# Kernel optimization log

Hardware: AMD Instinct MI355X
Metric: run time of the kernel (lower is better)

## Reference

```python
import jax, jax.numpy as jnp
import numpy as np

B = 32768
IN = 2
H = 512
OUT = 1
OM = 128   # output_module_size
HG = 128   # halt_gate_size
MAX_ITER = 32
EPS = 1e-3


def _w(k, shape, fan_in):
    bound = 1.0 / np.sqrt(fan_in)
    return jax.random.uniform(k, shape, jnp.float32, -bound, bound)


def setup_inputs() -> dict:
    key = jax.random.key(0)
    ks = jax.random.split(key, 32)
    d = {"x": jax.random.normal(ks[0], (B, IN), jnp.float32)}
    # four LSTM gates: input Linear(IN,H) and hidden Linear(H,H), each with bias
    names = ["i", "f", "c", "o"]
    for j, g in enumerate(names):
        d[f"W{g}_x"] = _w(ks[1 + 4 * j], (IN, H), IN)
        d[f"b{g}_x"] = _w(ks[2 + 4 * j], (H,), IN)
        d[f"W{g}_h"] = _w(ks[3 + 4 * j], (H, H), H)
        d[f"b{g}_h"] = _w(ks[4 + 4 * j], (H,), H)
    # halt gate: Linear(H,HG) -> ReLU -> Linear(HG,1) -> Sigmoid
    d["halt_W1"] = _w(ks[17], (H, HG), H)
    d["halt_b1"] = _w(ks[18], (HG,), H)
    d["halt_W2"] = _w(ks[19], (HG, 1), HG)
    d["halt_b2"] = _w(ks[20], (1,), HG)
    # output module: Linear(H,OM) -> ReLU -> Linear(OM,OM) -> Linear(OM,OUT) -> Sigmoid
    d["out_W1"] = _w(ks[21], (H, OM), H)
    d["out_b1"] = _w(ks[22], (OM,), H)
    d["out_W2"] = _w(ks[23], (OM, OM), OM)
    d["out_b2"] = _w(ks[24], (OM,), OM)
    d["out_W3"] = _w(ks[25], (OM, OUT), OM)
    d["out_b3"] = _w(ks[26], (OUT,), OM)
    return d


def _act_forward(x, Wi_x, bi_x, Wi_h, bi_h, Wf_x, bf_x, Wf_h, bf_h,
                 Wc_x, bc_x, Wc_h, bc_h, Wo_x, bo_x, Wo_h, bo_h,
                 halt_W1, halt_b1, halt_W2, halt_b2,
                 out_W1, out_b1, out_W2, out_b2, out_W3, out_b3):
    b = x.shape[0]
    # input projections are iteration-invariant: precompute once
    xi = x @ Wi_x + bi_x
    xf = x @ Wf_x + bf_x
    xc = x @ Wc_x + bc_x
    xo = x @ Wo_x + bo_x

    def step(carry, t):
        state, cell, p_sum, active, acc = carry
        i_g = jax.nn.sigmoid(xi + state @ Wi_h + bi_h)
        f_g = jax.nn.sigmoid(xf + state @ Wf_h + bf_h)
        c_g = jnp.tanh(xc + state @ Wc_h + bc_h)
        o_g = jax.nn.sigmoid(xo + state @ Wo_h + bo_h)
        am = active[:, None]
        new_cell = jnp.where(am, f_g * cell + i_g * c_g, cell)
        new_state = jnp.where(am, o_g * jnp.tanh(new_cell), state)
        # output head (inactive rows contribute zero weight below)
        h1 = jax.nn.relu(new_state @ out_W1 + out_b1)
        out = jax.nn.sigmoid((h1 @ out_W2 + out_b2) @ out_W3 + out_b3)  # [B,OUT]
        # halt probability
        hh = jax.nn.relu(new_state @ halt_W1 + halt_b1)
        halt = jax.nn.sigmoid(hh @ halt_W2 + halt_b2)[:, 0]  # [B]
        halt = jnp.where(active, halt, 0.0)
        p_new = p_sum + halt
        is_last = t == (MAX_ITER - 1)
        finished = (p_new >= 1.0 - EPS) | is_last
        adj = active & finished
        halt_adj = jnp.where(adj, halt + (1.0 - p_new), halt)
        p_new = jnp.where(adj, 1.0, p_new)
        acc = acc + out * halt_adj[:, None]
        active_new = active & jnp.logical_not(finished)
        return (new_state, new_cell, p_new, active_new, acc), None

    init = (
        jnp.zeros((b, H), jnp.float32),   # state
        jnp.zeros((b, H), jnp.float32),   # cell
        jnp.zeros((b,), jnp.float32),     # p_sum
        jnp.ones((b,), bool),             # active
        jnp.zeros((b, OUT), jnp.float32), # weighted-output accumulator
    )
    (state, cell, p_sum, active, acc), _ = jax.lax.scan(step, init, jnp.arange(MAX_ITER))
    return acc


def reference(x, Wi_x, bi_x, Wi_h, bi_h, Wf_x, bf_x, Wf_h, bf_h,
              Wc_x, bc_x, Wc_h, bc_h, Wo_x, bo_x, Wo_h, bo_h,
              halt_W1, halt_b1, halt_W2, halt_b2,
              out_W1, out_b1, out_W2, out_b2, out_W3, out_b3):
    return _act_forward(x, Wi_x, bi_x, Wi_h, bi_h, Wf_x, bf_x, Wf_h, bf_h,
                        Wc_x, bc_x, Wc_h, bc_h, Wo_x, bo_x, Wo_h, bo_h,
                        halt_W1, halt_b1, halt_W2, halt_b2,
                        out_W1, out_b1, out_W2, out_b2, out_W3, out_b3)
```

## Files before the change

### kernel.cpp

```cpp
#include <hip/hip_runtime.h>
#include <hip/hip_bf16.h>

#define KD   544
#define ASTR 552
#define RPB  64
#define THR  512
#define T1   3
#define NROW 32768

typedef __bf16 bf8 __attribute__((ext_vector_type(8)));
typedef float f32x4 __attribute__((ext_vector_type(4)));

__device__ __forceinline__ float sigm(float x)  { return 1.0f / (1.0f + __expf(-x)); }
__device__ __forceinline__ float tanh_(float x) { return 2.0f / (1.0f + __expf(-2.0f * x)) - 1.0f; }

__global__ void pack_all(const float* __restrict__ Wi_h, const float* __restrict__ Wf_h,
                         const float* __restrict__ Wc_h, const float* __restrict__ Wo_h,
                         const float* __restrict__ Wi_x, const float* __restrict__ Wf_x,
                         const float* __restrict__ Wc_x, const float* __restrict__ Wo_x,
                         const float* __restrict__ bi_x, const float* __restrict__ bf_x,
                         const float* __restrict__ bc_x, const float* __restrict__ bo_x,
                         const float* __restrict__ bi_h, const float* __restrict__ bf_h,
                         const float* __restrict__ bc_h, const float* __restrict__ bo_h,
                         const float* __restrict__ outW1, const float* __restrict__ outb1,
                         const float* __restrict__ haltW1, const float* __restrict__ haltb1,
                         const float* __restrict__ outW2, const float* __restrict__ outb2,
                         const float* __restrict__ outW3, const float* __restrict__ outb3,
                         __bf16* __restrict__ whT, __bf16* __restrict__ w1cat,
                         float* __restrict__ w23, float* __restrict__ b23,
                         int* __restrict__ cntp)
{
  int b = blockIdx.x;
  if (b < 4352) {
    int idx = b * 256 + threadIdx.x;
    int j = idx / KD, k = idx % KD;
    int g = j >> 9, c = j & 511;
    const float* Wh = (g == 0) ? Wi_h : (g == 1) ? Wf_h : (g == 2) ? Wc_h : Wo_h;
    const float* Wx = (g == 0) ? Wi_x : (g == 1) ? Wf_x : (g == 2) ? Wc_x : Wo_x;
    const float* bx = (g == 0) ? bi_x : (g == 1) ? bf_x : (g == 2) ? bc_x : bo_x;
    const float* bh = (g == 0) ? bi_h : (g == 1) ? bf_h : (g == 2) ? bc_h : bo_h;
    float v = 0.0f;
    if (k < 512)       v = Wh[k * 512 + c];
    else if (k == 512) v = Wx[c];
    else if (k == 513) v = Wx[512 + c];
    else if (k == 514) v = bx[c] + bh[c];
    whT[idx] = (__bf16)v;
  } else if (b < 4896) {
    int idx = (b - 4352) * 256 + threadIdx.x;
    int j = idx / KD, k = idx % KD;
    float v = 0.0f;
    if (j < 128) {
      if (k < 512)       v = outW1[k * 128 + j];
      else if (k == 514) v = outb1[j];
    } else {
      int jj = j - 128;
      if (k < 512)       v = haltW1[k * 128 + jj];
      else if (k == 514) v = haltb1[jj];
    }
    w1cat[idx] = (__bf16)v;
  } else {
    int c1 = threadIdx.x;
    if (c1 < 128) {
      float s = 0.0f;
      for (int c2 = 0; c2 < 128; ++c2) s += outW2[c1 * 128 + c2] * outW3[c2];
      w23[c1] = s;
    }
    if (c1 == 0) {
      float bb = 0.0f;
      for (int c2 = 0; c2 < 128; ++c2) bb += outb2[c2] * outW3[c2];
      b23[0] = bb + outb3[0];
      cntp[0] = 0;
    }
  }
}

template<bool P1>
__global__ __launch_bounds__(THR, 2) void act_pass(
    const float* __restrict__ x,
    const __bf16* __restrict__ whT,
    const __bf16* __restrict__ w1cat,
    const float* __restrict__ w23,
    const float* __restrict__ b23p,
    const float* __restrict__ haltW2,
    const float* __restrict__ haltb2,
    __bf16* __restrict__ sstate,
    __bf16* __restrict__ scell,
    float* __restrict__ spsum,
    float* __restrict__ saccum,
    int* __restrict__ sidx,
    int* __restrict__ cntp,
    float* __restrict__ out)
{
  int cnt_v = 0, sbase = 0;
  if constexpr (!P1) {
    cnt_v = cntp[0];
    sbase = blockIdx.x * RPB;
    if (sbase >= cnt_v) return;
  }

  __shared__ __align__(16) __bf16 Abuf[2][RPB][ASTR];
  __shared__ float wv[256];
  __shared__ float partials[8][RPB];
  __shared__ int anyact_s;
  __shared__ int rowslot[RPB];

  const int tid  = threadIdx.x;
  const int wave = tid >> 6;
  const int lane = tid & 63;
  const int lg   = lane >> 4;
  const int lc   = lane & 15;
  const int row0 = blockIdx.x * RPB;

  if (tid < 256) wv[tid] = (tid < 128) ? w23[tid] : haltW2[tid - 128];

  if constexpr (P1) {
    for (int w = tid; w < 2 * RPB * 69; w += THR) {
      int bb  = w / (RPB * 69);
      int rem = w - bb * (RPB * 69);
      int r   = rem / 69;
      int j   = rem - r * 69;
      bf8 v;
#pragma unroll
      for (int e = 0; e < 8; ++e) v[e] = (__bf16)0.0f;
      if (j == 64) {
        v[0] = (__bf16)x[(row0 + r) * 2 + 0];
        v[1] = (__bf16)x[(row0 + r) * 2 + 1];
        v[2] = (__bf16)1.0f;
      }
      *(bf8*)&Abuf[bb][r][j * 8] = v;
    }
  } else {
    for (int w = tid; w < RPB * 68; w += THR) {
      int r = w / 68, j = w - r * 68;
      int slot = sbase + r;
      bf8 v;
#pragma unroll
      for (int e = 0; e < 8; ++e) v[e] = (__bf16)0.0f;
      if (slot < cnt_v) v = *(const bf8*)(sstate + (size_t)slot * KD + j * 8);
      *(bf8*)&Abuf[0][r][j * 8] = v;
      if (j >= 64) *(bf8*)&Abuf[1][r][j * 8] = v;
    }
    for (int w = tid; w < RPB * 64; w += THR) {
      int r = w / 64, j = w - r * 64;
      int slot = sbase + r;
      bf8 v;
#pragma unroll
      for (int e = 0; e < 8; ++e) v[e] = (__bf16)0.0f;
      if (slot < cnt_v) v = *(const bf8*)(scell + (size_t)slot * 512 + j * 8);
      *(bf8*)&Abuf[1][r][j * 8] = v;
    }
  }
  if (tid == 0) anyact_s = 1;
  __syncthreads();

  float cell[4][4][4];
  if constexpr (P1) {
#pragma unroll
    for (int n = 0; n < 4; ++n)
#pragma unroll
      for (int m = 0; m < 4; ++m)
#pragma unroll
        for (int q = 0; q < 4; ++q) cell[n][m][q] = 0.0f;
  } else {
#pragma unroll
    for (int n = 0; n < 4; ++n)
#pragma unroll
      for (int m = 0; m < 4; ++m)
#pragma unroll
        for (int q = 0; q < 4; ++q)
          cell[n][m][q] = (float)Abuf[1][m * 16 + lg * 4 + q][wave * 64 + n * 16 + lc];
  }

  bool  valid, active;
  float p_sum, accum;
  int   oidx;
  if constexpr (P1) {
    valid = (tid < 64); active = valid;
    p_sum = 0.0f; accum = 0.0f; oidx = row0 + tid;
  } else {
    int slot = sbase + tid;
    valid = (tid < 64) && (slot < cnt_v);
    active = valid;
    p_sum = valid ? spsum[slot]  : 1.0f;
    accum = valid ? saccum[slot] : 0.0f;
    oidx  = valid ? sidx[slot]   : 0;
    __syncthreads();
  }

  const float b23 = b23p[0];
  const float bh2 = haltb2[0];
  const f32x4 zero4 = {0.0f, 0.0f, 0.0f, 0.0f};

  int cur = 0;
  const int T0 = P1 ? 0 : T1;
  const int TE = P1 ? T1 : 32;
  for (int t = T0; t < TE; ++t) {
    const int kstart = (P1 && t == 0) ? 16 : 0;
#pragma unroll
    for (int n = 0; n < 4; ++n) {
      const int colb = wave * 64 + n * 16 + lc;
      const __bf16* bp0 = whT + (size_t)(colb)        * KD + lg * 8;
      const __bf16* bp1 = whT + (size_t)(512  + colb) * KD + lg * 8;
      const __bf16* bp2 = whT + (size_t)(1024 + colb) * KD + lg * 8;
      const __bf16* bp3 = whT + (size_t)(1536 + colb) * KD + lg * 8;
      f32x4 acc[4][4];
#pragma unroll
      for (int g = 0; g < 4; ++g)
#pragma unroll
        for (int m = 0; m < 4; ++m) acc[g][m] = zero4;

      bf8 b0 = *(const bf8*)(bp0 + kstart * 32);
      bf8 b1 = *(const bf8*)(bp1 + kstart * 32);
      bf8 b2 = *(const bf8*)(bp2 + kstart * 32);
      bf8 b3 = *(const bf8*)(bp3 + kstart * 32);
#pragma unroll 1
      for (int kk = kstart; kk < 16; ++kk) {
        bf8 av[4];
#pragma unroll
        for (int m = 0; m < 4; ++m)
          av[m] = *(const bf8*)&Abuf[cur][m * 16 + lc][kk * 32 + lg * 8];
        bf8 nb0 = *(const bf8*)(bp0 + (kk + 1) * 32);
        bf8 nb1 = *(const bf8*)(bp1 + (kk + 1) * 32);
        bf8 nb2 = *(const bf8*)(bp2 + (kk + 1) * 32);
        bf8 nb3 = *(const bf8*)(bp3 + (kk + 1) * 32);
#pragma unroll
        for (int m = 0; m < 4; ++m) {
          acc[0][m] = __builtin_amdgcn_mfma_f32_16x16x32_bf16(av[m], b0, acc[0][m], 0, 0, 0);
          acc[1][m] = __builtin_amdgcn_mfma_f32_16x16x32_bf16(av[m], b1, acc[1][m], 0, 0, 0);
          acc[2][m] = __builtin_amdgcn_mfma_f32_16x16x32_bf16(av[m], b2, acc[2][m], 0, 0, 0);
          acc[3][m] = __builtin_amdgcn_mfma_f32_16x16x32_bf16(av[m], b3, acc[3][m], 0, 0, 0);
        }
        b0 = nb0; b1 = nb1; b2 = nb2; b3 = nb3;
      }
      {
        bf8 av[4];
#pragma unroll
        for (int m = 0; m < 4; ++m)
          av[m] = *(const bf8*)&Abuf[cur][m * 16 + lc][16 * 32 + lg * 8];
#pragma unroll
        for (int m = 0; m < 4; ++m) {
          acc[0][m] = __builtin_amdgcn_mfma_f32_16x16x32_bf16(av[m], b0, acc[0][m], 0, 0, 0);
          acc[1][m] = __builtin_amdgcn_mfma_f32_16x16x32_bf16(av[m], b1, acc[1][m], 0, 0, 0);
          acc[2][m] = __builtin_amdgcn_mfma_f32_16x16x32_bf16(av[m], b2, acc[2][m], 0, 0, 0);
          acc[3][m] = __builtin_amdgcn_mfma_f32_16x16x32_bf16(av[m], b3, acc[3][m], 0, 0, 0);
        }
      }
#pragma unroll
      for (int m = 0; m < 4; ++m) {
#pragma unroll
        for (int q = 0; q < 4; ++q) {
          float iv = sigm(acc[0][m][q]);
          float fv = sigm(acc[1][m][q]);
          float cv = tanh_(acc[2][m][q]);
          float ov = sigm(acc[3][m][q]);
          float cn = fv * cell[n][m][q] + iv * cv;
          cell[n][m][q] = cn;
          float h = ov * tanh_(cn);
          Abuf[cur ^ 1][m * 16 + lg * 4 + q][colb] = (__bf16)h;
        }
      }
    }
    __syncthreads();
    {
      const int jb0 = wave * 32 + lc;
      const __bf16* hp0 = w1cat + (size_t)jb0        * KD + lg * 8;
      const __bf16* hp1 = w1cat + (size_t)(jb0 + 16) * KD + lg * 8;
      f32x4 hacc[2][4];
#pragma unroll
      for (int n2 = 0; n2 < 2; ++n2)
#pragma unroll
        for (int m = 0; m < 4; ++m) hacc[n2][m] = zero4;
      bf8 hb0 = *(const bf8*)(hp0);
      bf8 hb1 = *(const bf8*)(hp1);
#pragma unroll 1
      for (int kk = 0; kk < 16; ++kk) {
        bf8 av[4];
#pragma unroll
        for (int m = 0; m < 4; ++m)
          av[m] = *(const bf8*)&Abuf[cur ^ 1][m * 16 + lc][kk * 32 + lg * 8];
        bf8 nb0 = *(const bf8*)(hp0 + (kk + 1) * 32);
        bf8 nb1 = *(const bf8*)(hp1 + (kk + 1) * 32);
#pragma unroll
        for (int m = 0; m < 4; ++m) {
          hacc[0][m] = __builtin_amdgcn_mfma_f32_16x16x32_bf16(av[m], hb0, hacc[0][m], 0, 0, 0);
          hacc[1][m] = __builtin_amdgcn_mfma_f32_16x16x32_bf16(av[m], hb1, hacc[1][m], 0, 0, 0);
        }
        hb0 = nb0; hb1 = nb1;
      }
      {
        bf8 av[4];
#pragma unroll
        for (int m = 0; m < 4; ++m)
          av[m] = *(const bf8*)&Abuf[cur ^ 1][m * 16 + lc][16 * 32 + lg * 8];
#pragma unroll
        for (int m = 0; m < 4; ++m) {
          hacc[0][m] = __builtin_amdgcn_mfma_f32_16x16x32_bf16(av[m], hb0, hacc[0][m], 0, 0, 0);
          hacc[1][m] = __builtin_amdgcn_mfma_f32_16x16x32_bf16(av[m], hb1, hacc[1][m], 0, 0, 0);
        }
      }
      const float wv0 = wv[wave * 32 + lc];
      const float wv1 = wv[wave * 32 + 16 + lc];
#pragma unroll
      for (int m = 0; m < 4; ++m) {
#pragma unroll
        for (int q = 0; q < 4; ++q) {
          float s = fmaxf(hacc[0][m][q], 0.0f) * wv0 + fmaxf(hacc[1][m][q], 0.0f) * wv1;
          s += __shfl_xor(s, 1, 64);
          s += __shfl_xor(s, 2, 64);
          s += __shfl_xor(s, 4, 64);
          s += __shfl_xor(s, 8, 64);
          if (lc == 0) partials[wave][m * 16 + lg * 4 + q] = s;
        }
      }
    }
    __syncthreads();
    if (tid < 64) {
      float od = partials[0][tid] + partials[1][tid] + partials[2][tid] + partials[3][tid] + b23;
      float hd = partials[4][tid] + partials[5][tid] + partials[6][tid] + partials[7][tid] + bh2;
      float outv  = sigm(od);
      float haltv = sigm(hd);
      if (active) {
        float pn  = p_sum + haltv;
        bool  fin = (pn >= 0.999f) || (t == 31);
        accum += outv * (fin ? (haltv + (1.0f - pn)) : haltv);
        p_sum  = fin ? 1.0f : pn;
        active = !fin;
      }
      unsigned long long mk = __ballot(active);
      if (tid == 0) anyact_s = (mk != 0ull) ? 1 : 0;
    }
    __syncthreads();
    if (!anyact_s) break;
    cur ^= 1;
  }

  if constexpr (P1) {
    if (tid < 64) {
      unsigned long long mk = __ballot(active);
      int base = 0;
      if (lane == 0 && mk) base = atomicAdd(cntp, __popcll(mk));
      base = __shfl(base, 0, 64);
      int rank = __popcll(mk & ((1ull << lane) - 1ull));
      int slot = active ? (base + rank) : -1;
      rowslot[tid] = slot;
      if (active) {
        spsum[slot]  = p_sum;
        saccum[slot] = accum;
        sidx[slot]   = oidx;
      } else {
        out[oidx] = accum;
      }
      if (tid == 0) anyact_s = (mk != 0ull) ? 1 : 0;
    }
    __syncthreads();
    if (anyact_s) {
#pragma unroll
      for (int n = 0; n < 4; ++n)
#pragma unroll
        for (int m = 0; m < 4; ++m)
#pragma unroll
          for (int q = 0; q < 4; ++q)
            Abuf[cur ^ 1][m * 16 + lg * 4 + q][wave * 64 + n * 16 + lc] = (__bf16)cell[n][m][q];
      __syncthreads();
      for (int w = tid; w < RPB * 132; w += THR) {
        int r = w / 132, j = w - r * 132;
        int slot = rowslot[r];
        if (slot < 0) continue;
        if (j < 68)
          *(bf8*)(sstate + (size_t)slot * KD + j * 8) = *(const bf8*)&Abuf[cur][r][j * 8];
        else {
          int jj = j - 68;
          *(bf8*)(scell + (size_t)slot * 512 + jj * 8) = *(const bf8*)&Abuf[cur ^ 1][r][jj * 8];
        }
      }
    }
  } else {
    if (valid) out[oidx] = accum;
  }
}

extern "C" void kernel_launch(void* const* d_in, const int* in_sizes, int n_in,
                              void* d_out, int out_size, void* d_ws, size_t ws_size,
                              hipStream_t stream) {
  const float* x     = (const float*)d_in[0];
  const float* Wi_x  = (const float*)d_in[1];
  const float* bi_x  = (const float*)d_in[2];
  const float* Wi_h  = (const float*)d_in[3];
  const float* bi_h  = (const float*)d_in[4];
  const float* Wf_x  = (const float*)d_in[5];
  const float* bf_x  = (const float*)d_in[6];
  const float* Wf_h  = (const float*)d_in[7];
  const float* bf_h  = (const float*)d_in[8];
  const float* Wc_x  = (const float*)d_in[9];
  const float* bc_x  = (const float*)d_in[10];
  const float* Wc_h  = (const float*)d_in[11];
  const float* bc_h  = (const float*)d_in[12];
  const float* Wo_x  = (const float*)d_in[13];
  const float* bo_x  = (const float*)d_in[14];
  const float* Wo_h  = (const float*)d_in[15];
  const float* bo_h  = (const float*)d_in[16];
  const float* hW1   = (const float*)d_in[17];
  const float* hb1   = (const float*)d_in[18];
  const float* hW2   = (const float*)d_in[19];
  const float* hb2   = (const float*)d_in[20];
  const float* oW1   = (const float*)d_in[21];
  const float* ob1   = (const float*)d_in[22];
  const float* oW2   = (const float*)d_in[23];
  const float* ob2   = (const float*)d_in[24];
  const float* oW3   = (const float*)d_in[25];
  const float* ob3   = (const float*)d_in[26];

  char* p = (char*)d_ws;
  __bf16* whT   = (__bf16*)p;                       p += (size_t)2048 * KD * 2;
  __bf16* w1cat = (__bf16*)p;                       p += (size_t)256 * KD * 2;
  float*  w23   = (float*)p;                        p += 512;
  float*  b23   = (float*)p;                        p += 16;
  int*    cnt   = (int*)p;                          p += 240;
  __bf16* sstate= (__bf16*)p;                       p += (size_t)NROW * KD * 2;
  __bf16* scell = (__bf16*)p;                       p += (size_t)NROW * 512 * 2;
  float*  spsum = (float*)p;                        p += (size_t)NROW * 4;
  float*  saccum= (float*)p;                        p += (size_t)NROW * 4;
  int*    sidx  = (int*)p;                          p += (size_t)NROW * 4;

  pack_all<<<dim3(4897), dim3(256), 0, stream>>>(
      Wi_h, Wf_h, Wc_h, Wo_h, Wi_x, Wf_x, Wc_x, Wo_x,
      bi_x, bf_x, bc_x, bo_x, bi_h, bf_h, bc_h, bo_h,
      oW1, ob1, hW1, hb1, oW2, ob2, oW3, ob3,
      whT, w1cat, w23, b23, cnt);
  act_pass<true><<<dim3(NROW / RPB), dim3(THR), 0, stream>>>(
      x, whT, w1cat, w23, b23, hW2, hb2,
      sstate, scell, spsum, saccum, sidx, cnt, (float*)d_out);
  act_pass<false><<<dim3(NROW / RPB), dim3(THR), 0, stream>>>(
      x, whT, w1cat, w23, b23, hW2, hb2,
      sstate, scell, spsum, saccum, sidx, cnt, (float*)d_out);
}
```

Before: 407.3 us.

## Tile-transpose weight packing via LDS and deepen MFMA operand prefetch to two stages

The weight-packing kernel now transposes 64x64 tiles through shared memory, giving coalesced reads and vectorized bf16 writes, and launches far fewer blocks. The gate and head GEMM loops now prefetch B operands two K-steps ahead and A operands one step ahead, with the tail step folded into the main loop. This is meant to cut the strided-read cost of packing and to hide global and LDS load latency behind the MFMAs. The cost is more live registers, which could hurt occupancy at two blocks per CU, plus redundant clamped loads at the tail.

```diff
diff --git a/kernel.cpp b/kernel.cpp
--- a/kernel.cpp
+++ b/kernel.cpp
@@ -30,36 +30,84 @@
                          float* __restrict__ w23, float* __restrict__ b23,
                          int* __restrict__ cntp)
 {
-  int b = blockIdx.x;
-  if (b < 4352) {
-    int idx = b * 256 + threadIdx.x;
-    int j = idx / KD, k = idx % KD;
-    int g = j >> 9, c = j & 511;
+  __shared__ float tile[64][65];
+  const int b = blockIdx.x;
+  const int tid = threadIdx.x;
+
+  if (b < 256) {
+    const int g = b >> 6, ct = (b >> 3) & 7, kt = b & 7;
+    const int c0 = ct * 64, k0 = kt * 64;
     const float* Wh = (g == 0) ? Wi_h : (g == 1) ? Wf_h : (g == 2) ? Wc_h : Wo_h;
+    const int ty = tid >> 6, tx = tid & 63;
+#pragma unroll
+    for (int r = 0; r < 16; ++r) {
+      int kl = r * 4 + ty;
+      tile[kl][tx] = Wh[(size_t)(k0 + kl) * 512 + c0 + tx];
+    }
+    __syncthreads();
+    const int jj = tid >> 2, kq = tid & 3;
+    bf8 lo, hi;
+#pragma unroll
+    for (int i = 0; i < 8; ++i) lo[i] = (__bf16)tile[kq * 16 + i][jj];
+#pragma unroll
+    for (int i = 0; i < 8; ++i) hi[i] = (__bf16)tile[kq * 16 + 8 + i][jj];
+    __bf16* dst = whT + (size_t)(g * 512 + c0 + jj) * KD + k0 + kq * 16;
+    *(bf8*)dst = lo;
+    *(bf8*)(dst + 8) = hi;
+  } else if (b < 288) {
+    const int b2 = b - 256;
+    const int g = b2 >> 3, ct = b2 & 7;
     const float* Wx = (g == 0) ? Wi_x : (g == 1) ? Wf_x : (g == 2) ? Wc_x : Wo_x;
     const float* bx = (g == 0) ? bi_x : (g == 1) ? bf_x : (g == 2) ? bc_x : bo_x;
     const float* bh = (g == 0) ? bi_h : (g == 1) ? bf_h : (g == 2) ? bc_h : bo_h;
-    float v = 0.0f;
-    if (k < 512)       v = Wh[k * 512 + c];
-    else if (k == 512) v = Wx[c];
-    else if (k == 513) v = Wx[512 + c];
-    else if (k == 514) v = bx[c] + bh[c];
-    whT[idx] = (__bf16)v;
-  } else if (b < 4896) {
-    int idx = (b - 4352) * 256 + threadIdx.x;
-    int j = idx / KD, k = idx % KD;
-    float v = 0.0f;
-    if (j < 128) {
-      if (k < 512)       v = outW1[k * 128 + j];
-      else if (k == 514) v = outb1[j];
-    } else {
-      int jj = j - 128;
-      if (k < 512)       v = haltW1[k * 128 + jj];
-      else if (k == 514) v = haltb1[jj];
-    }
-    w1cat[idx] = (__bf16)v;
+    const int jj = tid >> 2, kq = tid & 3;
+    const int c = ct * 64 + jj;
+    bf8 v;
+#pragma unroll
+    for (int i = 0; i < 8; ++i) {
+      int k = 512 + kq * 8 + i;
+      float f = 0.0f;
+      if (k == 512)      f = Wx[c];
+      else if (k == 513) f = Wx[512 + c];
+      else if (k == 514) f = bx[c] + bh[c];
+      v[i] = (__bf16)f;
+    }
+    *(bf8*)(whT + (size_t)(g * 512 + c) * KD + 512 + kq * 8) = v;
+  } else if (b < 320) {
+    const int b2 = b - 288;
+    const int src = b2 >> 4, jt = (b2 >> 3) & 1, kt = b2 & 7;
+    const float* W = src ? haltW1 : outW1;
+    const int c0 = jt * 64, k0 = kt * 64;
+    const int ty = tid >> 6, tx = tid & 63;
+#pragma unroll
+    for (int r = 0; r < 16; ++r) {
+      int kl = r * 4 + ty;
+      tile[kl][tx] = W[(size_t)(k0 + kl) * 128 + c0 + tx];
+    }
+    __syncthreads();
+    const int jj = tid >> 2, kq = tid & 3;
+    bf8 lo, hi;
+#pragma unroll
+    for (int i = 0; i < 8; ++i) lo[i] = (__bf16)tile[kq * 16 + i][jj];
+#pragma unroll
+    for (int i = 0; i < 8; ++i) hi[i] = (__bf16)tile[kq * 16 + 8 + i][jj];
+    __bf16* dst = w1cat + (size_t)(src * 128 + c0 + jj) * KD + k0 + kq * 16;
+    *(bf8*)dst = lo;
+    *(bf8*)(dst + 8) = hi;
+  } else if (b < 324) {
+    const int b2 = b - 320;
+    const int jj = tid >> 2, kq = tid & 3;
+    const int j = b2 * 64 + jj;
+    const float bias = (j < 128) ? outb1[j] : haltb1[j - 128];
+    bf8 v;
+#pragma unroll
+    for (int i = 0; i < 8; ++i) {
+      int k = 512 + kq * 8 + i;
+      v[i] = (__bf16)((k == 514) ? bias : 0.0f);
+    }
+    *(bf8*)(w1cat + (size_t)j * KD + 512 + kq * 8) = v;
   } else {
-    int c1 = threadIdx.x;
+    const int c1 = tid;
     if (c1 < 128) {
       float s = 0.0f;
       for (int c2 = 0; c2 < 128; ++c2) s += outW2[c1 * 128 + c2] * outW3[c2];
@@ -199,51 +247,49 @@
 #pragma unroll
     for (int n = 0; n < 4; ++n) {
       const int colb = wave * 64 + n * 16 + lc;
-      const __bf16* bp0 = whT + (size_t)(colb)        * KD + lg * 8;
-      const __bf16* bp1 = whT + (size_t)(512  + colb) * KD + lg * 8;
-      const __bf16* bp2 = whT + (size_t)(1024 + colb) * KD + lg * 8;
-      const __bf16* bp3 = whT + (size_t)(1536 + colb) * KD + lg * 8;
+      const __bf16* bp[4];
+      bp[0] = whT + (size_t)colb * KD + lg * 8;
+      bp[1] = bp[0] + (size_t)512  * KD;
+      bp[2] = bp[0] + (size_t)1024 * KD;
+      bp[3] = bp[0] + (size_t)1536 * KD;
       f32x4 acc[4][4];
 #pragma unroll
       for (int g = 0; g < 4; ++g)
 #pragma unroll
         for (int m = 0; m < 4; ++m) acc[g][m] = zero4;
 
-      bf8 b0 = *(const bf8*)(bp0 + kstart * 32);
-      bf8 b1 = *(const bf8*)(bp1 + kstart * 32);
-      bf8 b2 = *(const bf8*)(bp2 + kstart * 32);
-      bf8 b3 = *(const bf8*)(bp3 + kstart * 32);
+      bf8 bA[4], bB[4], avA[4];
+      const int k1 = (kstart < 16) ? kstart + 1 : 16;
+#pragma unroll
+      for (int g = 0; g < 4; ++g) {
+        bA[g] = *(const bf8*)(bp[g] + kstart * 32);
+        bB[g] = *(const bf8*)(bp[g] + k1 * 32);
+      }
+#pragma unroll
+      for (int m = 0; m < 4; ++m)
+        avA[m] = *(const bf8*)&Abuf[cur][m * 16 + lc][kstart * 32 + lg * 8];
+
 #pragma unroll 1
-      for (int kk = kstart; kk < 16; ++kk) {
-        bf8 av[4];
+      for (int kk = kstart; kk <= 16; ++kk) {
+        const int kp2 = (kk + 2 <= 16) ? kk + 2 : 16;
+        const int kp1 = (kk + 1 <= 16) ? kk + 1 : 16;
+        bf8 bC[4], avB[4];
+#pragma unroll
+        for (int g = 0; g < 4; ++g) bC[g] = *(const bf8*)(bp[g] + kp2 * 32);
 #pragma unroll
         for (int m = 0; m < 4; ++m)
-          av[m] = *(const bf8*)&Abuf[cur][m * 16 + lc][kk * 32 + lg * 8];
-        bf8 nb0 = *(const bf8*)(bp0 + (kk + 1) * 32);
-        bf8 nb1 = *(const bf8*)(bp1 + (kk + 1) * 32);
-        bf8 nb2 = *(const bf8*)(bp2 + (kk + 1) * 32);
-        bf8 nb3 = *(const bf8*)(bp3 + (kk + 1) * 32);
+          avB[m] = *(const bf8*)&Abuf[cur][m * 16 + lc][kp1 * 32 + lg * 8];
 #pragma unroll
         for (int m = 0; m < 4; ++m) {
-          acc[0][m] = __builtin_amdgcn_mfma_f32_16x16x32_bf16(av[m], b0, acc[0][m], 0, 0, 0);
-          acc[1][m] = __builtin_amdgcn_mfma_f32_16x16x32_bf16(av[m], b1, acc[1][m], 0, 0, 0);
-          acc[2][m] = __builtin_amdgcn_mfma_f32_16x16x32_bf16(av[m], b2, acc[2][m], 0, 0, 0);
-          acc[3][m] = __builtin_amdgcn_mfma_f32_16x16x32_bf16(av[m], b3, acc[3][m], 0, 0, 0);
+          acc[0][m] = __builtin_amdgcn_mfma_f32_16x16x32_bf16(avA[m], bA[0], acc[0][m], 0, 0, 0);
+          acc[1][m] = __builtin_amdgcn_mfma_f32_16x16x32_bf16(avA[m], bA[1], acc[1][m], 0, 0, 0);
+          acc[2][m] = __builtin_amdgcn_mfma_f32_16x16x32_bf16(avA[m], bA[2], acc[2][m], 0, 0, 0);
+          acc[3][m] = __builtin_amdgcn_mfma_f32_16x16x32_bf16(avA[m], bA[3], acc[3][m], 0, 0, 0);
         }
-        b0 = nb0; b1 = nb1; b2 = nb2; b3 = nb3;
-      }
-      {
-        bf8 av[4];
-#pragma unroll
-        for (int m = 0; m < 4; ++m)
-          av[m] = *(const bf8*)&Abuf[cur][m * 16 + lc][16 * 32 + lg * 8];
-#pragma unroll
-        for (int m = 0; m < 4; ++m) {
-          acc[0][m] = __builtin_amdgcn_mfma_f32_16x16x32_bf16(av[m], b0, acc[0][m], 0, 0, 0);
-          acc[1][m] = __builtin_amdgcn_mfma_f32_16x16x32_bf16(av[m], b1, acc[1][m], 0, 0, 0);
-          acc[2][m] = __builtin_amdgcn_mfma_f32_16x16x32_bf16(av[m], b2, acc[2][m], 0, 0, 0);
-          acc[3][m] = __builtin_amdgcn_mfma_f32_16x16x32_bf16(av[m], b3, acc[3][m], 0, 0, 0);
-        }
+#pragma unroll
+        for (int g = 0; g < 4; ++g) { bA[g] = bB[g]; bB[g] = bC[g]; }
+#pragma unroll
+        for (int m = 0; m < 4; ++m) avA[m] = avB[m];
       }
 #pragma unroll
       for (int m = 0; m < 4; ++m) {
@@ -263,40 +309,44 @@
     __syncthreads();
     {
       const int jb0 = wave * 32 + lc;
-      const __bf16* hp0 = w1cat + (size_t)jb0        * KD + lg * 8;
-      const __bf16* hp1 = w1cat + (size_t)(jb0 + 16) * KD + lg * 8;
+      const __bf16* hp[2];
+      hp[0] = w1cat + (size_t)jb0 * KD + lg * 8;
+      hp[1] = hp[0] + (size_t)16 * KD;
       f32x4 hacc[2][4];
 #pragma unroll
       for (int n2 = 0; n2 < 2; ++n2)
 #pragma unroll
         for (int m = 0; m < 4; ++m) hacc[n2][m] = zero4;
-      bf8 hb0 = *(const bf8*)(hp0);
-      bf8 hb1 = *(const bf8*)(hp1);
+
+      bf8 hA[2], hB[2], avA[4];
+#pragma unroll
+      for (int g = 0; g < 2; ++g) {
+        hA[g] = *(const bf8*)(hp[g]);
+        hB[g] = *(const bf8*)(hp[g] + 32);
+      }
+#pragma unroll
+      for (int m = 0; m < 4; ++m)
+        avA[m] = *(const bf8*)&Abuf[cur ^ 1][m * 16 + lc][lg * 8];
+
 #pragma unroll 1
-      for (int kk = 0; kk < 16; ++kk) {
-        bf8 av[4];
+      for (int kk = 0; kk <= 16; ++kk) {
+        const int kp2 = (kk + 2 <= 16) ? kk + 2 : 16;
+        const int kp1 = (kk + 1 <= 16) ? kk + 1 : 16;
+        bf8 hC[2], avB[4];
+#pragma unroll
+        for (int g = 0; g < 2; ++g) hC[g] = *(const bf8*)(hp[g] + kp2 * 32);
 #pragma unroll
         for (int m = 0; m < 4; ++m)
-          av[m] = *(const bf8*)&Abuf[cur ^ 1][m * 16 + lc][kk * 32 + lg * 8];
-        bf8 nb0 = *(const bf8*)(hp0 + (kk + 1) * 32);
-        bf8 nb1 = *(const bf8*)(hp1 + (kk + 1) * 32);
+          avB[m] = *(const bf8*)&Abuf[cur ^ 1][m * 16 + lc][kp1 * 32 + lg * 8];
 #pragma unroll
         for (int m = 0; m < 4; ++m) {
-          hacc[0][m] = __builtin_amdgcn_mfma_f32_16x16x32_bf16(av[m], hb0, hacc[0][m], 0, 0, 0);
-          hacc[1][m] = __builtin_amdgcn_mfma_f32_16x16x32_bf16(av[m], hb1, hacc[1][m], 0, 0, 0);
+          hacc[0][m] = __builtin_amdgcn_mfma_f32_16x16x32_bf16(avA[m], hA[0], hacc[0][m], 0, 0, 0);
+          hacc[1][m] = __builtin_amdgcn_mfma_f32_16x16x32_bf16(avA[m], hA[1], hacc[1][m], 0, 0, 0);
         }
-        hb0 = nb0; hb1 = nb1;
-      }
-      {
-        bf8 av[4];
-#pragma unroll
-        for (int m = 0; m < 4; ++m)
-          av[m] = *(const bf8*)&Abuf[cur ^ 1][m * 16 + lc][16 * 32 + lg * 8];
-#pragma unroll
-        for (int m = 0; m < 4; ++m) {
-          hacc[0][m] = __builtin_amdgcn_mfma_f32_16x16x32_bf16(av[m], hb0, hacc[0][m], 0, 0, 0);
-          hacc[1][m] = __builtin_amdgcn_mfma_f32_16x16x32_bf16(av[m], hb1, hacc[1][m], 0, 0, 0);
-        }
+#pragma unroll
+        for (int g = 0; g < 2; ++g) { hA[g] = hB[g]; hB[g] = hC[g]; }
+#pragma unroll
+        for (int m = 0; m < 4; ++m) avA[m] = avB[m];
       }
       const float wv0 = wv[wave * 32 + lc];
       const float wv1 = wv[wave * 32 + 16 + lc];
@@ -422,7 +472,7 @@
   float*  saccum= (float*)p;                        p += (size_t)NROW * 4;
   int*    sidx  = (int*)p;                          p += (size_t)NROW * 4;
 
-  pack_all<<<dim3(4897), dim3(256), 0, stream>>>(
+  pack_all<<<dim3(325), dim3(256), 0, stream>>>(
       Wi_h, Wf_h, Wc_h, Wo_h, Wi_x, Wf_x, Wc_x, Wo_x,
       bi_x, bf_x, bc_x, bo_x, bi_h, bf_h, bc_h, bo_h,
       oW1, ob1, hW1, hb1, oW2, ob2, oW3, ob3,
```

After: 415.4 us. No clear change (+2.0%).

## Pre-swizzle LSTM and head weights into MFMA fragment order for coalesced loads

Applied to the files above, without the earlier changes.

The packing kernel now writes the recurrent and head weights in a tiled layout. Each 16-column by 32-k MFMA B fragment is stored as 64 contiguous 16-byte lane chunks, so a wave's weight fetch in the main loop becomes one fully coalesced 1 KB read instead of strided row reads. The pack itself is rewritten to go through a shared-memory transpose tile, which cuts the launch from thousands of blocks to a few hundred and reads the fp32 source coalesced. The trade-off is more complex index math in the packing and addressing code, and correctness depends on the fragment mapping matching exactly.

```diff
diff --git a/kernel.cpp b/kernel.cpp
--- a/kernel.cpp
+++ b/kernel.cpp
@@ -26,40 +26,104 @@
                          const float* __restrict__ haltW1, const float* __restrict__ haltb1,
                          const float* __restrict__ outW2, const float* __restrict__ outb2,
                          const float* __restrict__ outW3, const float* __restrict__ outb3,
-                         __bf16* __restrict__ whT, __bf16* __restrict__ w1cat,
+                         __bf16* __restrict__ whT2, __bf16* __restrict__ w1cat2,
                          float* __restrict__ w23, float* __restrict__ b23,
                          int* __restrict__ cntp)
 {
-  int b = blockIdx.x;
-  if (b < 4352) {
-    int idx = b * 256 + threadIdx.x;
-    int j = idx / KD, k = idx % KD;
-    int g = j >> 9, c = j & 511;
+  __shared__ float tile[64][65];
+  const int b = blockIdx.x;
+  const int tid = threadIdx.x;
+
+  if (b < 256) {
+    const int g = b >> 6, ct4 = (b >> 3) & 7, kt2 = b & 7;
+    const int c0 = ct4 * 64, k0 = kt2 * 64;
     const float* Wh = (g == 0) ? Wi_h : (g == 1) ? Wf_h : (g == 2) ? Wc_h : Wo_h;
+    const int ty = tid >> 6, tx = tid & 63;
+#pragma unroll
+    for (int r = 0; r < 16; ++r) {
+      int kl = r * 4 + ty;
+      tile[kl][tx] = Wh[(size_t)(k0 + kl) * 512 + c0 + tx];
+    }
+    __syncthreads();
+#pragma unroll
+    for (int h = 0; h < 2; ++h) {
+      int chunk = tid + h * 256;
+      int ct_l = chunk >> 7;
+      int kt_l = (chunk >> 6) & 1;
+      int l    = chunk & 63;
+      int cl = ct_l * 16 + (l & 15);
+      int kb = kt_l * 32 + (l >> 4) * 8;
+      bf8 v;
+#pragma unroll
+      for (int e = 0; e < 8; ++e) v[e] = (__bf16)tile[kb + e][cl];
+      int ct_g = g * 32 + ct4 * 4 + ct_l;
+      int kt_g = kt2 * 2 + kt_l;
+      *(bf8*)(whT2 + ((size_t)(ct_g * 17 + kt_g) * 64 + l) * 8) = v;
+    }
+  } else if (b < 288) {
+    const int b2 = b - 256;
+    const int g = b2 >> 3, ct4 = b2 & 7;
     const float* Wx = (g == 0) ? Wi_x : (g == 1) ? Wf_x : (g == 2) ? Wc_x : Wo_x;
     const float* bx = (g == 0) ? bi_x : (g == 1) ? bf_x : (g == 2) ? bc_x : bo_x;
     const float* bh = (g == 0) ? bi_h : (g == 1) ? bf_h : (g == 2) ? bc_h : bo_h;
-    float v = 0.0f;
-    if (k < 512)       v = Wh[k * 512 + c];
-    else if (k == 512) v = Wx[c];
-    else if (k == 513) v = Wx[512 + c];
-    else if (k == 514) v = bx[c] + bh[c];
-    whT[idx] = (__bf16)v;
-  } else if (b < 4896) {
-    int idx = (b - 4352) * 256 + threadIdx.x;
-    int j = idx / KD, k = idx % KD;
-    float v = 0.0f;
-    if (j < 128) {
-      if (k < 512)       v = outW1[k * 128 + j];
-      else if (k == 514) v = outb1[j];
-    } else {
-      int jj = j - 128;
-      if (k < 512)       v = haltW1[k * 128 + jj];
-      else if (k == 514) v = haltb1[jj];
-    }
-    w1cat[idx] = (__bf16)v;
+    const int ct_l = tid >> 6, l = tid & 63;
+    const int c = ct4 * 64 + ct_l * 16 + (l & 15);
+    const int kb = (l >> 4) * 8;
+    bf8 v;
+#pragma unroll
+    for (int e = 0; e < 8; ++e) {
+      int ka = kb + e;
+      float f = 0.0f;
+      if (ka == 0)      f = Wx[c];
+      else if (ka == 1) f = Wx[512 + c];
+      else if (ka == 2) f = bx[c] + bh[c];
+      v[e] = (__bf16)f;
+    }
+    int ct_g = g * 32 + ct4 * 4 + ct_l;
+    *(bf8*)(whT2 + ((size_t)(ct_g * 17 + 16) * 64 + l) * 8) = v;
+  } else if (b < 320) {
+    const int b2 = b - 288;
+    const int src = b2 >> 4, jt = (b2 >> 3) & 1, kt2 = b2 & 7;
+    const float* W = src ? haltW1 : outW1;
+    const int c0 = jt * 64, k0 = kt2 * 64;
+    const int ty = tid >> 6, tx = tid & 63;
+#pragma unroll
+    for (int r = 0; r < 16; ++r) {
+      int kl = r * 4 + ty;
+      tile[kl][tx] = W[(size_t)(k0 + kl) * 128 + c0 + tx];
+    }
+    __syncthreads();
+#pragma unroll
+    for (int h = 0; h < 2; ++h) {
+      int chunk = tid + h * 256;
+      int ct_l = chunk >> 7;
+      int kt_l = (chunk >> 6) & 1;
+      int l    = chunk & 63;
+      int cl = ct_l * 16 + (l & 15);
+      int kb = kt_l * 32 + (l >> 4) * 8;
+      bf8 v;
+#pragma unroll
+      for (int e = 0; e < 8; ++e) v[e] = (__bf16)tile[kb + e][cl];
+      int ct_g = src * 8 + jt * 4 + ct_l;
+      int kt_g = kt2 * 2 + kt_l;
+      *(bf8*)(w1cat2 + ((size_t)(ct_g * 17 + kt_g) * 64 + l) * 8) = v;
+    }
+  } else if (b < 324) {
+    const int grp = b - 320;
+    const int ct_l = tid >> 6, l = tid & 63;
+    const int j = grp * 64 + ct_l * 16 + (l & 15);
+    const float bias = (j < 128) ? outb1[j] : haltb1[j - 128];
+    const int kb = (l >> 4) * 8;
+    bf8 v;
+#pragma unroll
+    for (int e = 0; e < 8; ++e) {
+      int ka = kb + e;
+      v[e] = (__bf16)((ka == 2) ? bias : 0.0f);
+    }
+    int ct_g = grp * 4 + ct_l;
+    *(bf8*)(w1cat2 + ((size_t)(ct_g * 17 + 16) * 64 + l) * 8) = v;
   } else {
-    int c1 = threadIdx.x;
+    const int c1 = tid;
     if (c1 < 128) {
       float s = 0.0f;
       for (int c2 = 0; c2 < 128; ++c2) s += outW2[c1 * 128 + c2] * outW3[c2];
@@ -77,8 +141,8 @@
 template<bool P1>
 __global__ __launch_bounds__(THR, 2) void act_pass(
     const float* __restrict__ x,
-    const __bf16* __restrict__ whT,
-    const __bf16* __restrict__ w1cat,
+    const __bf16* __restrict__ whT2,
+    const __bf16* __restrict__ w1cat2,
     const float* __restrict__ w23,
     const float* __restrict__ b23p,
     const float* __restrict__ haltW2,
@@ -199,30 +263,31 @@
 #pragma unroll
     for (int n = 0; n < 4; ++n) {
       const int colb = wave * 64 + n * 16 + lc;
-      const __bf16* bp0 = whT + (size_t)(colb)        * KD + lg * 8;
-      const __bf16* bp1 = whT + (size_t)(512  + colb) * KD + lg * 8;
-      const __bf16* bp2 = whT + (size_t)(1024 + colb) * KD + lg * 8;
-      const __bf16* bp3 = whT + (size_t)(1536 + colb) * KD + lg * 8;
+      const int ctn = wave * 4 + n;
+      const __bf16* bp0 = whT2 + ((size_t)((0 * 32 + ctn) * 17) * 64 + lane) * 8;
+      const __bf16* bp1 = whT2 + ((size_t)((1 * 32 + ctn) * 17) * 64 + lane) * 8;
+      const __bf16* bp2 = whT2 + ((size_t)((2 * 32 + ctn) * 17) * 64 + lane) * 8;
+      const __bf16* bp3 = whT2 + ((size_t)((3 * 32 + ctn) * 17) * 64 + lane) * 8;
       f32x4 acc[4][4];
 #pragma unroll
       for (int g = 0; g < 4; ++g)
 #pragma unroll
         for (int m = 0; m < 4; ++m) acc[g][m] = zero4;
 
-      bf8 b0 = *(const bf8*)(bp0 + kstart * 32);
-      bf8 b1 = *(const bf8*)(bp1 + kstart * 32);
-      bf8 b2 = *(const bf8*)(bp2 + kstart * 32);
-      bf8 b3 = *(const bf8*)(bp3 + kstart * 32);
+      bf8 b0 = *(const bf8*)(bp0 + kstart * 512);
+      bf8 b1 = *(const bf8*)(bp1 + kstart * 512);
+      bf8 b2 = *(const bf8*)(bp2 + kstart * 512);
+      bf8 b3 = *(const bf8*)(bp3 + kstart * 512);
 #pragma unroll 1
       for (int kk = kstart; kk < 16; ++kk) {
         bf8 av[4];
 #pragma unroll
         for (int m = 0; m < 4; ++m)
           av[m] = *(const bf8*)&Abuf[cur][m * 16 + lc][kk * 32 + lg * 8];
-        bf8 nb0 = *(const bf8*)(bp0 + (kk + 1) * 32);
-        bf8 nb1 = *(const bf8*)(bp1 + (kk + 1) * 32);
-        bf8 nb2 = *(const bf8*)(bp2 + (kk + 1) * 32);
-        bf8 nb3 = *(const bf8*)(bp3 + (kk + 1) * 32);
+        bf8 nb0 = *(const bf8*)(bp0 + (kk + 1) * 512);
+        bf8 nb1 = *(const bf8*)(bp1 + (kk + 1) * 512);
+        bf8 nb2 = *(const bf8*)(bp2 + (kk + 1) * 512);
+        bf8 nb3 = *(const bf8*)(bp3 + (kk + 1) * 512);
 #pragma unroll
         for (int m = 0; m < 4; ++m) {
           acc[0][m] = __builtin_amdgcn_mfma_f32_16x16x32_bf16(av[m], b0, acc[0][m], 0, 0, 0);
@@ -262,9 +327,8 @@
     }
     __syncthreads();
     {
-      const int jb0 = wave * 32 + lc;
-      const __bf16* hp0 = w1cat + (size_t)jb0        * KD + lg * 8;
-      const __bf16* hp1 = w1cat + (size_t)(jb0 + 16) * KD + lg * 8;
+      const __bf16* hp0 = w1cat2 + ((size_t)((wave * 2 + 0) * 17) * 64 + lane) * 8;
+      const __bf16* hp1 = w1cat2 + ((size_t)((wave * 2 + 1) * 17) * 64 + lane) * 8;
       f32x4 hacc[2][4];
 #pragma unroll
       for (int n2 = 0; n2 < 2; ++n2)
@@ -278,8 +342,8 @@
 #pragma unroll
         for (int m = 0; m < 4; ++m)
           av[m] = *(const bf8*)&Abuf[cur ^ 1][m * 16 + lc][kk * 32 + lg * 8];
-        bf8 nb0 = *(const bf8*)(hp0 + (kk + 1) * 32);
-        bf8 nb1 = *(const bf8*)(hp1 + (kk + 1) * 32);
+        bf8 nb0 = *(const bf8*)(hp0 + (kk + 1) * 512);
+        bf8 nb1 = *(const bf8*)(hp1 + (kk + 1) * 512);
 #pragma unroll
         for (int m = 0; m < 4; ++m) {
           hacc[0][m] = __builtin_amdgcn_mfma_f32_16x16x32_bf16(av[m], hb0, hacc[0][m], 0, 0, 0);
@@ -411,8 +475,8 @@
   const float* ob3   = (const float*)d_in[26];
 
   char* p = (char*)d_ws;
-  __bf16* whT   = (__bf16*)p;                       p += (size_t)2048 * KD * 2;
-  __bf16* w1cat = (__bf16*)p;                       p += (size_t)256 * KD * 2;
+  __bf16* whT2  = (__bf16*)p;                       p += (size_t)2048 * KD * 2;
+  __bf16* w1cat2= (__bf16*)p;                       p += (size_t)256 * KD * 2;
   float*  w23   = (float*)p;                        p += 512;
   float*  b23   = (float*)p;                        p += 16;
   int*    cnt   = (int*)p;                          p += 240;
@@ -422,15 +486,15 @@
   float*  saccum= (float*)p;                        p += (size_t)NROW * 4;
   int*    sidx  = (int*)p;                          p += (size_t)NROW * 4;
 
-  pack_all<<<dim3(4897), dim3(256), 0, stream>>>(
+  pack_all<<<dim3(325), dim3(256), 0, stream>>>(
       Wi_h, Wf_h, Wc_h, Wo_h, Wi_x, Wf_x, Wc_x, Wo_x,
       bi_x, bf_x, bc_x, bo_x, bi_h, bf_h, bc_h, bo_h,
       oW1, ob1, hW1, hb1, oW2, ob2, oW3, ob3,
-      whT, w1cat, w23, b23, cnt);
+      whT2, w1cat2, w23, b23, cnt);
   act_pass<true><<<dim3(NROW / RPB), dim3(THR), 0, stream>>>(
-      x, whT, w1cat, w23, b23, hW2, hb2,
+      x, whT2, w1cat2, w23, b23, hW2, hb2,
       sstate, scell, spsum, saccum, sidx, cnt, (float*)d_out);
   act_pass<false><<<dim3(NROW / RPB), dim3(THR), 0, stream>>>(
-      x, whT, w1cat, w23, b23, hW2, hb2,
+      x, whT2, w1cat2, w23, b23, hW2, hb2,
       sstate, scell, spsum, saccum, sidx, cnt, (float*)d_out);
 }
```

Result: faster. 370.2 us (-9.1%).
